# Performance work log

Measured on AMD Instinct MI355X. Metric: run time of the kernel, lower is better.

Reference implementation:

```python
import jax, jax.numpy as jnp
import numpy as np

V, DH, E, KV = 30, 512, 256, 128  # vocab, decoder hidden, embed (=2*KV, tied), key/value dim
B, T, L = 256, 800, 300
SOS = 0


def _lstm_cell(x, h, c, w_ih, w_hh, b_ih, b_hh):
    g = x @ w_ih.T + b_ih + h @ w_hh.T + b_hh
    i, f, gg, o = jnp.split(g, 4, axis=-1)
    i, f, o = jax.nn.sigmoid(i), jax.nn.sigmoid(f), jax.nn.sigmoid(o)
    c2 = f * c + i * jnp.tanh(gg)
    return o * jnp.tanh(c2), c2


def setup_inputs() -> dict:
    key = jax.random.key(0)
    ks = jax.random.split(key, 12)
    emb = 0.1 * jax.random.normal(ks[0], (V, E), jnp.float32)
    emb = emb.at[0].set(0.0)  # padding_idx=0
    return {
        "key_enc": jax.random.normal(ks[1], (B, T, KV), jnp.float32),
        "value": jax.random.normal(ks[2], (B, T, KV), jnp.float32),
        "encoder_len": jax.random.randint(ks[3], (B,), 100, T + 1, jnp.int32),
        "y": jax.random.randint(ks[4], (B, L), 0, V, jnp.int64),
        "embedding": emb,  # also the tied character_prob weight (V, 2*KV)
        "w_ih1": 0.05 * jax.random.normal(ks[5], (4 * DH, E + KV), jnp.float32),
        "w_hh1": 0.05 * jax.random.normal(ks[6], (4 * DH, DH), jnp.float32),
        "b_ih1": jnp.zeros((4 * DH,), jnp.float32),
        "b_hh1": jnp.zeros((4 * DH,), jnp.float32),
        "w_ih2": 0.05 * jax.random.normal(ks[7], (4 * KV, DH), jnp.float32),
        "w_hh2": 0.05 * jax.random.normal(ks[8], (4 * KV, KV), jnp.float32),
        "b_ih2": jnp.zeros((4 * KV,), jnp.float32),
        "b_hh2": jnp.zeros((4 * KV,), jnp.float32),
        "out_bias": jnp.zeros((V,), jnp.float32),
    }


def reference(key_enc, value, encoder_len, y, embedding,
              w_ih1, w_hh1, b_ih1, b_hh1, w_ih2, w_hh2, b_ih2, b_hh2, out_bias):
    Bb, Tt, _ = key_enc.shape
    max_len = y.shape[1]
    valid = jnp.arange(Tt)[None, :] < encoder_len[:, None]  # (B, T)

    # teacher-forced embeddings: <sos> then y[:, :-1]
    sos = jnp.broadcast_to(embedding[SOS], (Bb, E))
    embeds = jnp.concatenate([sos[:, None, :], embedding[y[:, :-1]]], axis=1)  # (B, L, E)
    embeds = jnp.transpose(embeds, (1, 0, 2))  # (L, B, E)

    z1 = jnp.zeros((Bb, DH), key_enc.dtype)
    z2 = jnp.zeros((Bb, KV), key_enc.dtype)
    init = (z1, z1, z2, z2, value[:, 0, :])

    def step(carry, emb):
        h1, c1, h2, c2, ctx = carry
        x = jnp.concatenate([emb, ctx], axis=1)
        h1, c1 = _lstm_cell(x, h1, c1, w_ih1, w_hh1, b_ih1, b_hh1)
        h2, c2 = _lstm_cell(h1, h2, c2, w_ih2, w_hh2, b_ih2, b_hh2)
        q = h2  # (B, KV)
        energy = jnp.einsum('btk,bk->bt', key_enc, q)
        energy = jnp.where(valid, energy, -1e9)
        attn = jax.nn.softmax(energy, axis=-1)
        ctx = jnp.einsum('bt,btk->bk', attn, value)
        pred = jnp.concatenate([q, ctx], axis=1) @ embedding.T + out_bias  # tied weights
        return (h1, c1, h2, c2, ctx), (pred, attn[0])

    _, (preds, attn_plot) = jax.lax.scan(step, init, embeds)
    predictions = jnp.transpose(preds, (1, 0, 2))  # (B, L, V)
    return predictions, attn_plot  # attn_plot: (L, T)
```

## Files before the change

kernel.cpp:

```cpp
#include <hip/hip_runtime.h>
#include <cstddef>

#define NV   30
#define NDH  512
#define NE   256
#define NKV  128
#define NB   256
#define NT   800
#define NL   300
#define NKX  896

#define PRED_SIZE (NB*NL*NV)

typedef float v4f __attribute__((ext_vector_type(4)));
typedef float v2f __attribute__((ext_vector_type(2)));
typedef short bf16x8 __attribute__((ext_vector_type(8)));
typedef unsigned short ushort_t;

#define OFF_XT  0
#define OFF_C1  229376
#define OFF_H2  360448
#define OFF_C2  425984
#define OFF_GP  458752
#define OFF_BP  1507328
#define OFF_XB  2031616
#define OFF_WF  2293760

struct DecParams {
  const float* key; const float* val; const int* elen; const int* y;
  const float* emb;
  const float* wi1; const float* wh1; const float* bi1; const float* bh1;
  const float* wi2; const float* wh2; const float* bi2; const float* bh2;
  const float* ob;
  float* out; float* ws;
};

__device__ __forceinline__ float sigm(float x)  { return 1.0f/(1.0f + __expf(-x)); }
__device__ __forceinline__ float tanh_f(float x){ return 1.0f - 2.0f/(__expf(2.0f*x)+1.0f); }

__device__ __forceinline__ ushort_t bf16_rne(float x){
  union { float f; unsigned u; } v; v.f = x;
  unsigned r = v.u + 0x7FFFu + ((v.u >> 16) & 1u);
  return (ushort_t)(r >> 16);
}
__device__ __forceinline__ float bf16_to_f(ushort_t h){
  union { float f; unsigned u; } v; v.u = ((unsigned)h) << 16;
  return v.f;
}

__global__ void __launch_bounds__(256)
k_init(DecParams P)
{
  const int idx = blockIdx.x * 256 + threadIdx.x;
  P.ws[idx] = 0.0f;
}

__global__ void __launch_bounds__(256)
k_initX(DecParams P)
{
  const int b = blockIdx.x, tid = threadIdx.x;
  ushort_t* xb = (ushort_t*)(P.ws + OFF_XB);
  ushort_t* xbh = xb;
  ushort_t* xbl = xb + 256*1024;
#pragma unroll
  for (int i = 0; i < 4; ++i) {
    const int k = i*256 + tid;
    float v = 0.0f;
    if (k >= 256 && k < 384) v = P.val[(size_t)b*NT*NKV + (k - 256)];
    ushort_t hi = bf16_rne(v);
    ushort_t lo = bf16_rne(v - bf16_to_f(hi));
    xbh[(size_t)b*1024 + k] = hi;
    xbl[(size_t)b*1024 + k] = lo;
  }
}

__global__ void __launch_bounds__(256)
k_initW(DecParams P)
{
  const int r = blockIdx.x;
  const int tid = threadIdx.x;
  ushort_t* wf = (ushort_t*)(P.ws + OFF_WF);
  const int rt = r >> 4;
#pragma unroll
  for (int i = 0; i < 4; ++i) {
    const int k = i*256 + tid;
    if (k < NKX) {
      const float w = (k < 384) ? P.wi1[(size_t)r*384 + k]
                                : P.wh1[(size_t)r*512 + (k - 384)];
      ushort_t hi = bf16_rne(w);
      ushort_t lo = bf16_rne(w - bf16_to_f(hi));
      const int kc = k >> 5;
      const int lane = (r & 15) | (((k >> 3) & 3) << 4);
      const int e = k & 7;
      const size_t base = ((((size_t)rt)*28 + kc)*64 + lane)*8 + e;
      wf[base] = hi;
      wf[(size_t)128*28*64*8 + base] = lo;
    }
  }
}

__global__ void __launch_bounds__(256)
k_stepA(DecParams P)
{
  __shared__ ushort_t xs[2][64][72];
  const int tid = threadIdx.x, bid = blockIdx.x;
  const int mt = bid & 31, nt = (bid >> 5) & 3, kt = bid >> 7;
  const int w = tid >> 6, lane = tid & 63;
  const int rt16 = mt*4 + w;
  const int b0 = nt * 64;

  const ushort_t* Wf = (const ushort_t*)(P.ws + OFF_WF);
  const ushort_t* Xb = (const ushort_t*)(P.ws + OFF_XB);
  float* Gp = P.ws + OFF_GP;

  v4f acc[4];
#pragma unroll
  for (int i = 0; i < 4; ++i) acc[i] = (v4f)0.0f;

  const int srow = tid >> 2, skq = (tid & 3) * 16;
  const int lr = lane & 15, lk8 = (lane >> 4) * 8;

#pragma unroll 1
  for (int p = 0; p < 7; ++p) {
    const int kg = kt*448 + p*64;
    __syncthreads();
    {
      const ushort_t* s0 = Xb + (size_t)(b0 + srow)*1024 + kg + skq;
      const ushort_t* s1 = s0 + (size_t)256*1024;
      *(bf16x8*)&xs[0][srow][skq]     = *(const bf16x8*)(s0);
      *(bf16x8*)&xs[0][srow][skq + 8] = *(const bf16x8*)(s0 + 8);
      *(bf16x8*)&xs[1][srow][skq]     = *(const bf16x8*)(s1);
      *(bf16x8*)&xs[1][srow][skq + 8] = *(const bf16x8*)(s1 + 8);
    }
    __syncthreads();
#pragma unroll
    for (int kc2 = 0; kc2 < 2; ++kc2) {
      const int kcg = (kg >> 5) + kc2;
      bf16x8 ah = *(const bf16x8*)(Wf + ((((size_t)0*128 + rt16)*28 + kcg)*64 + lane)*8);
      bf16x8 al = *(const bf16x8*)(Wf + ((((size_t)1*128 + rt16)*28 + kcg)*64 + lane)*8);
      const int lk = kc2*32 + lk8;
#pragma unroll
      for (int ct = 0; ct < 4; ++ct) {
        bf16x8 bh = *(const bf16x8*)&xs[0][ct*16 + lr][lk];
        bf16x8 bl = *(const bf16x8*)&xs[1][ct*16 + lr][lk];
        acc[ct] = __builtin_amdgcn_mfma_f32_16x16x32_bf16(ah, bh, acc[ct], 0, 0, 0);
        acc[ct] = __builtin_amdgcn_mfma_f32_16x16x32_bf16(ah, bl, acc[ct], 0, 0, 0);
        acc[ct] = __builtin_amdgcn_mfma_f32_16x16x32_bf16(al, bh, acc[ct], 0, 0, 0);
      }
    }
  }
  const int rg = (lane >> 4) * 4;
  const int r0 = rt16 * 16;
#pragma unroll
  for (int ct = 0; ct < 4; ++ct)
#pragma unroll
    for (int j = 0; j < 4; ++j)
      Gp[((size_t)kt*2048 + r0 + rg + j)*256 + b0 + ct*16 + lr] = acc[ct][j];
}

__global__ void __launch_bounds__(256)
k_afin(DecParams P)
{
  const int j = blockIdx.x;
  const int b = threadIdx.x;
  const float* Gp = P.ws + OFF_GP;
  float* Xt = P.ws + OFF_XT;
  float* C1 = P.ws + OFF_C1;
  ushort_t* xb = (ushort_t*)(P.ws + OFF_XB);

  float s[4];
#pragma unroll
  for (int g = 0; g < 4; ++g) {
    const size_t base = ((size_t)g*512 + j)*256 + b;
    s[g] = Gp[base] + Gp[(size_t)2048*256 + base]
         + P.bi1[g*512 + j] + P.bh1[g*512 + j];
  }
  const float ig = sigm(s[0]);
  const float fg = sigm(s[1]);
  const float gg = tanh_f(s[2]);
  const float og = sigm(s[3]);
  const float cn = fg * C1[(size_t)j*256 + b] + ig * gg;
  C1[(size_t)j*256 + b] = cn;
  const float h = og * tanh_f(cn);
  Xt[(size_t)(384 + j)*256 + b] = h;
  ushort_t hi = bf16_rne(h);
  ushort_t lo = bf16_rne(h - bf16_to_f(hi));
  xb[(size_t)b*1024 + 384 + j] = hi;
  xb[(size_t)256*1024 + (size_t)b*1024 + 384 + j] = lo;
}

__global__ void __launch_bounds__(256)
k_stepB(DecParams P, int t)
{
  __shared__ float xs2[32][36];
  __shared__ float wr2[32][36];
  const int tid = threadIdx.x;
  const int bid = blockIdx.x;
  const int bt = bid & 7, jt = (bid >> 3) & 15, kt = bid >> 7;
  const int b0 = bt * 32, r0 = jt * 32;
  const int bq = tid & 15, rq = tid >> 4;

  const float* Xt = P.ws + OFF_XT;
  const float* H2p = P.ws + OFF_H2 + (size_t)(t & 1) * 32768;
  float* Bp = P.ws + OFF_BP;

  v2f acc[2] = {(v2f)0.0f, (v2f)0.0f};

  const int kx_ld = tid >> 3, bx4 = (tid & 7) * 4;
  const int rw_ld = tid >> 3, kw4 = (tid & 7) * 4;

#pragma unroll 1
  for (int cc = 0; cc < 5; ++cc) {
    const int kg0 = kt * 160 + cc * 32;
    __syncthreads();
    {
      const int kg = kg0 + kx_ld;
      const float* src = (kg < 512) ? (Xt + (size_t)(384 + kg)*256 + b0 + bx4)
                                    : (H2p + (size_t)(kg - 512)*256 + b0 + bx4);
      *(v4f*)&xs2[kx_ld][bx4] = *(const v4f*)src;
    }
    {
      const int row = r0 + rw_ld;
      const int kg = kg0 + kw4;
      const float* src = (kg < 512) ? (P.wi2 + (size_t)row*512 + kg)
                                    : (P.wh2 + (size_t)row*128 + (kg - 512));
      *(v4f*)&wr2[rw_ld][kw4] = *(const v4f*)src;
    }
    __syncthreads();
#pragma unroll
    for (int p = 0; p < 16; ++p) {
      v2f x0 = *(const v2f*)&xs2[p*2+0][bq*2];
      v2f x1 = *(const v2f*)&xs2[p*2+1][bq*2];
#pragma unroll
      for (int ri = 0; ri < 2; ++ri) {
        v2f w = *(const v2f*)&wr2[rq*2+ri][p*2];
        acc[ri] += w[0]*x0 + w[1]*x1;
      }
    }
  }
#pragma unroll
  for (int bi = 0; bi < 2; ++bi) {
    v2f st; st[0] = acc[0][bi]; st[1] = acc[1][bi];
    *(v2f*)&Bp[((size_t)kt*256 + b0 + bq*2 + bi)*512 + r0 + rq*2] = st;
  }
}

__global__ void __launch_bounds__(512)
k_stepC(DecParams P, int t)
{
  __shared__ float e[NT];
  __shared__ float g2s[512];
  __shared__ float qc[256];
  __shared__ float red[16];
  __shared__ float ctxp[16][132];

  const int tid = threadIdx.x;
  const int b = blockIdx.x;
  const int len = P.elen[b];
  float* C2 = P.ws + OFF_C2;
  const float* Bp = P.ws + OFF_BP;
  float* H2n = P.ws + OFF_H2 + (size_t)((t + 1) & 1) * 32768;
  ushort_t* xbh = (ushort_t*)(P.ws + OFF_XB);
  ushort_t* xbl = xbh + (size_t)256*1024;

  {
    const int r = tid;
    const size_t base = (size_t)b*512 + r;
    float s = Bp[base] + Bp[256*512 + base] + Bp[2*256*512 + base] + Bp[3*256*512 + base]
            + P.bi2[r] + P.bh2[r];
    g2s[r] = s;
  }
  __syncthreads();
  if (tid < 128) {
    const int j2 = tid;
    const float ig = sigm(g2s[j2]);
    const float fg = sigm(g2s[128 + j2]);
    const float gg = tanh_f(g2s[256 + j2]);
    const float og = sigm(g2s[384 + j2]);
    const float cn = fg * C2[(size_t)b*128 + j2] + ig * gg;
    C2[(size_t)b*128 + j2] = cn;
    const float h = og * tanh_f(cn);
    qc[j2] = h;
    H2n[(size_t)j2*256 + b] = h;
  }
  __syncthreads();

  const int lg = tid & 15, grp = tid >> 4;
  const v4f qa = *(const v4f*)&qc[lg*8];
  const v4f qb = *(const v4f*)&qc[lg*8 + 4];
  const v4f* kb = (const v4f*)(P.key + (size_t)b*NT*NKV);
#pragma unroll 1
  for (int s = 0; s < 13; ++s) {
    const int ta = s*64 + grp, tb = ta + 32;
    float pa = 0.0f, pb = 0.0f;
    if (ta < len) {
      v4f k0 = kb[(size_t)ta*32 + lg*2], k1 = kb[(size_t)ta*32 + lg*2 + 1];
      v4f d = k0*qa + k1*qb; pa = d[0]+d[1]+d[2]+d[3];
    }
    if (tb < len) {
      v4f k0 = kb[(size_t)tb*32 + lg*2], k1 = kb[(size_t)tb*32 + lg*2 + 1];
      v4f d = k0*qa + k1*qb; pb = d[0]+d[1]+d[2]+d[3];
    }
    pa += __shfl_xor(pa, 1); pb += __shfl_xor(pb, 1);
    pa += __shfl_xor(pa, 2); pb += __shfl_xor(pb, 2);
    pa += __shfl_xor(pa, 4); pb += __shfl_xor(pb, 4);
    pa += __shfl_xor(pa, 8); pb += __shfl_xor(pb, 8);
    if (lg == 0) {
      if (ta < len) e[ta] = pa;
      if (tb < len) e[tb] = pb;
    }
  }
  for (int tt = len + tid; tt < NT; tt += 512) e[tt] = -1e9f;
  __syncthreads();

  const int wid = tid >> 6;
  const float x0 = e[tid];
  const float x1 = (tid < NT - 512) ? e[512 + tid] : -3.0e38f;
  float m = fmaxf(x0, x1);
  m = fmaxf(m, __shfl_xor(m, 1));  m = fmaxf(m, __shfl_xor(m, 2));
  m = fmaxf(m, __shfl_xor(m, 4));  m = fmaxf(m, __shfl_xor(m, 8));
  m = fmaxf(m, __shfl_xor(m, 16)); m = fmaxf(m, __shfl_xor(m, 32));
  if ((tid & 63) == 0) red[wid] = m;
  __syncthreads();
  m = red[0];
#pragma unroll
  for (int i = 1; i < 8; ++i) m = fmaxf(m, red[i]);
  const float p0 = __expf(x0 - m);
  const float p1 = (tid < NT - 512) ? __expf(x1 - m) : 0.0f;
  float ss = p0 + p1;
  ss += __shfl_xor(ss, 1);  ss += __shfl_xor(ss, 2);  ss += __shfl_xor(ss, 4);
  ss += __shfl_xor(ss, 8);  ss += __shfl_xor(ss, 16); ss += __shfl_xor(ss, 32);
  if ((tid & 63) == 0) red[8 + wid] = ss;
  __syncthreads();
  float S = red[8];
#pragma unroll
  for (int i = 1; i < 8; ++i) S += red[8 + i];
  const float inv = 1.0f / S;
  e[tid] = p0 * inv;
  if (tid < NT - 512) e[512 + tid] = p1 * inv;
  if (b == 0) {
    P.out[PRED_SIZE + (size_t)t*NT + tid] = p0 * inv;
    if (tid < NT - 512) P.out[PRED_SIZE + (size_t)t*NT + 512 + tid] = p1 * inv;
  }
  __syncthreads();

  {
    const int kq = tid & 31, tq = tid >> 5;
    const v4f* vb = (const v4f*)(P.val + (size_t)b*NT*NKV);
    v4f a4 = (v4f)0.0f, a42 = (v4f)0.0f;
    int tt = tq;
    for (; tt + 16 < len; tt += 32) {
      a4  += e[tt]      * vb[(size_t)tt*32 + kq];
      a42 += e[tt + 16] * vb[(size_t)(tt + 16)*32 + kq];
    }
    if (tt < len) a4 += e[tt] * vb[(size_t)tt*32 + kq];
    a4 += a42;
    *(v4f*)&ctxp[tq][kq*4] = a4;
  }
  __syncthreads();
  if (tid < 128) {
    const int k = tid;
    float c = 0.0f;
#pragma unroll
    for (int r = 0; r < 16; ++r) c += ctxp[r][k];
    qc[128 + k] = c;
    ushort_t hi = bf16_rne(c);
    ushort_t lo = bf16_rne(c - bf16_to_f(hi));
    xbh[(size_t)b*1024 + 256 + k] = hi;
    xbl[(size_t)b*1024 + 256 + k] = lo;
  }
  __syncthreads();

  {
    const int vv = tid >> 4, lg16 = tid & 15;
    if (vv < NV) {
      const v4f* er = (const v4f*)(P.emb + (size_t)vv*NE + lg16*16);
      const v4f* qr = (const v4f*)&qc[lg16*16];
      v4f s4 = er[0]*qr[0] + er[1]*qr[1] + er[2]*qr[2] + er[3]*qr[3];
      float p = s4[0] + s4[1] + s4[2] + s4[3];
      p += __shfl_xor(p, 1); p += __shfl_xor(p, 2);
      p += __shfl_xor(p, 4); p += __shfl_xor(p, 8);
      if (lg16 == 0) P.out[((size_t)b*NL + t)*NV + vv] = p + P.ob[vv];
    }
  }

  if (tid < 256) {
    const int tok = P.y[(size_t)b*NL + t];
    const float x = P.emb[(size_t)tok*NE + tid];
    ushort_t hi = bf16_rne(x);
    ushort_t lo = bf16_rne(x - bf16_to_f(hi));
    xbh[(size_t)b*1024 + tid] = hi;
    xbl[(size_t)b*1024 + tid] = lo;
  }
}

extern "C" void kernel_launch(void* const* d_in, const int* in_sizes, int n_in,
                              void* d_out, int out_size, void* d_ws, size_t ws_size,
                              hipStream_t stream) {
  (void)in_sizes; (void)n_in; (void)out_size; (void)ws_size;
  DecParams P;
  P.key  = (const float*)d_in[0];
  P.val  = (const float*)d_in[1];
  P.elen = (const int*)d_in[2];
  P.y    = (const int*)d_in[3];
  P.emb  = (const float*)d_in[4];
  P.wi1  = (const float*)d_in[5];
  P.wh1  = (const float*)d_in[6];
  P.bi1  = (const float*)d_in[7];
  P.bh1  = (const float*)d_in[8];
  P.wi2  = (const float*)d_in[9];
  P.wh2  = (const float*)d_in[10];
  P.bi2  = (const float*)d_in[11];
  P.bh2  = (const float*)d_in[12];
  P.ob   = (const float*)d_in[13];
  P.out  = (float*)d_out;
  P.ws   = (float*)d_ws;

  hipLaunchKernelGGL(k_init,  dim3(1792), dim3(256), 0, stream, P);
  hipLaunchKernelGGL(k_initX, dim3(256),  dim3(256), 0, stream, P);
  hipLaunchKernelGGL(k_initW, dim3(2048), dim3(256), 0, stream, P);
  for (int t = 0; t < NL; ++t) {
    hipLaunchKernelGGL(k_stepA, dim3(256), dim3(256), 0, stream, P);
    hipLaunchKernelGGL(k_afin,  dim3(512), dim3(256), 0, stream, P);
    hipLaunchKernelGGL(k_stepB, dim3(512), dim3(256), 0, stream, P, t);
    hipLaunchKernelGGL(k_stepC, dim3(NB),  dim3(512), 0, stream, P, t);
  }
}
```

Baseline: 14.94 ms.

## Fuse LSTM gate epilogues into MFMA GEMMs and move layer-2 GEMM to split-bf16 MFMA

Layer-1 GEMM no longer splits K across blocks. Each block now computes all four gates for a 16-unit by 32-batch tile and applies the LSTM cell in-kernel, which removes the separate k_afin launch and the partial-sum buffer. Layer-2 is reworked the same way: its weights are prepacked to hi/lo bf16 fragments and it uses 3-pass MFMA, and the layer-2 cell update moves out of stepC into stepB. This cuts per-step launches from four to three and drops a global round-trip. The trade-off is fewer blocks per GEMM (256 and 64), with longer K loops per block.

```diff
diff --git a/kernel.cpp b/kernel.cpp
--- a/kernel.cpp
+++ b/kernel.cpp
@@ -13,18 +13,21 @@
 #define PRED_SIZE (NB*NL*NV)
 
 typedef float v4f __attribute__((ext_vector_type(4)));
-typedef float v2f __attribute__((ext_vector_type(2)));
 typedef short bf16x8 __attribute__((ext_vector_type(8)));
 typedef unsigned short ushort_t;
 
-#define OFF_XT  0
-#define OFF_C1  229376
-#define OFF_H2  360448
-#define OFF_C2  425984
-#define OFF_GP  458752
-#define OFF_BP  1507328
-#define OFF_XB  2031616
-#define OFF_WF  2293760
+#define OFF_C1   0
+#define OFF_C2   131072
+#define OFF_H2F  163840
+#define OFF_XB   196608
+#define OFF_XH2  458752
+#define OFF_WF   524288
+#define OFF_WF2  2359296
+#define OFF_BS1  2686976
+#define OFF_BS2  2689024
+
+#define WF_PL   ((size_t)128*28*64*8)
+#define WF2_PL  ((size_t)32*20*64*8)
 
 struct DecParams {
   const float* key; const float* val; const int* elen; const int* y;
@@ -51,26 +54,21 @@
 __global__ void __launch_bounds__(256)
 k_init(DecParams P)
 {
-  const int idx = blockIdx.x * 256 + threadIdx.x;
-  P.ws[idx] = 0.0f;
+  P.ws[blockIdx.x * 256 + threadIdx.x] = 0.0f;
 }
 
 __global__ void __launch_bounds__(256)
 k_initX(DecParams P)
 {
   const int b = blockIdx.x, tid = threadIdx.x;
-  ushort_t* xb = (ushort_t*)(P.ws + OFF_XB);
-  ushort_t* xbh = xb;
-  ushort_t* xbl = xb + 256*1024;
-#pragma unroll
-  for (int i = 0; i < 4; ++i) {
-    const int k = i*256 + tid;
-    float v = 0.0f;
-    if (k >= 256 && k < 384) v = P.val[(size_t)b*NT*NKV + (k - 256)];
-    ushort_t hi = bf16_rne(v);
-    ushort_t lo = bf16_rne(v - bf16_to_f(hi));
-    xbh[(size_t)b*1024 + k] = hi;
-    xbl[(size_t)b*1024 + k] = lo;
+  if (tid < 128) {
+    ushort_t* xbh = (ushort_t*)(P.ws + OFF_XB);
+    ushort_t* xbl = xbh + (size_t)256*1024;
+    const float v = P.val[(size_t)b*NT*NKV + tid];
+    const ushort_t hi = bf16_rne(v);
+    const ushort_t lo = bf16_rne(v - bf16_to_f(hi));
+    xbh[(size_t)b*1024 + 256 + tid] = hi;
+    xbl[(size_t)b*1024 + 256 + tid] = lo;
   }
 }
 
@@ -87,60 +85,86 @@
     if (k < NKX) {
       const float w = (k < 384) ? P.wi1[(size_t)r*384 + k]
                                 : P.wh1[(size_t)r*512 + (k - 384)];
-      ushort_t hi = bf16_rne(w);
-      ushort_t lo = bf16_rne(w - bf16_to_f(hi));
+      const ushort_t hi = bf16_rne(w);
+      const ushort_t lo = bf16_rne(w - bf16_to_f(hi));
       const int kc = k >> 5;
       const int lane = (r & 15) | (((k >> 3) & 3) << 4);
       const int e = k & 7;
       const size_t base = ((((size_t)rt)*28 + kc)*64 + lane)*8 + e;
       wf[base] = hi;
-      wf[(size_t)128*28*64*8 + base] = lo;
-    }
-  }
+      wf[WF_PL + base] = lo;
+    }
+  }
+  if (tid == 0) P.ws[OFF_BS1 + r] = P.bi1[r] + P.bh1[r];
+}
+
+__global__ void __launch_bounds__(256)
+k_initW2(DecParams P)
+{
+  const int r = blockIdx.x;
+  const int tid = threadIdx.x;
+  ushort_t* wf = (ushort_t*)(P.ws + OFF_WF2);
+  const int rt = r >> 4;
+#pragma unroll
+  for (int i = 0; i < 3; ++i) {
+    const int k = i*256 + tid;
+    if (k < 640) {
+      const float w = (k < 512) ? P.wi2[(size_t)r*512 + k]
+                                : P.wh2[(size_t)r*128 + (k - 512)];
+      const ushort_t hi = bf16_rne(w);
+      const ushort_t lo = bf16_rne(w - bf16_to_f(hi));
+      const int kc = k >> 5;
+      const int lane = (r & 15) | (((k >> 3) & 3) << 4);
+      const int e = k & 7;
+      const size_t base = ((((size_t)rt)*20 + kc)*64 + lane)*8 + e;
+      wf[base] = hi;
+      wf[WF2_PL + base] = lo;
+    }
+  }
+  if (tid == 0) P.ws[OFF_BS2 + r] = P.bi2[r] + P.bh2[r];
 }
 
 __global__ void __launch_bounds__(256)
 k_stepA(DecParams P)
 {
-  __shared__ ushort_t xs[2][64][72];
+  __shared__ ushort_t xs[2][32][136];
+  __shared__ float gbuf[4][16][33];
   const int tid = threadIdx.x, bid = blockIdx.x;
-  const int mt = bid & 31, nt = (bid >> 5) & 3, kt = bid >> 7;
+  const int mt = bid & 31, nt = bid >> 5;
+  const int b0 = nt * 32, j0 = mt * 16;
   const int w = tid >> 6, lane = tid & 63;
-  const int rt16 = mt*4 + w;
-  const int b0 = nt * 64;
-
-  const ushort_t* Wf = (const ushort_t*)(P.ws + OFF_WF);
-  const ushort_t* Xb = (const ushort_t*)(P.ws + OFF_XB);
-  float* Gp = P.ws + OFF_GP;
-
-  v4f acc[4];
-#pragma unroll
-  for (int i = 0; i < 4; ++i) acc[i] = (v4f)0.0f;
-
-  const int srow = tid >> 2, skq = (tid & 3) * 16;
+  const int rt16 = w*32 + mt;
+
+  const ushort_t* Wf  = (const ushort_t*)(P.ws + OFF_WF);
+  const ushort_t* XbH = (const ushort_t*)(P.ws + OFF_XB);
+  const ushort_t* XbL = XbH + (size_t)256*1024;
+  float* C1 = P.ws + OFF_C1;
+  const float* BS1 = P.ws + OFF_BS1;
+
+  v4f acc[2] = {(v4f)0.0f, (v4f)0.0f};
+  const int srow = tid >> 3, sk = (tid & 7) * 16;
   const int lr = lane & 15, lk8 = (lane >> 4) * 8;
 
 #pragma unroll 1
   for (int p = 0; p < 7; ++p) {
-    const int kg = kt*448 + p*64;
     __syncthreads();
     {
-      const ushort_t* s0 = Xb + (size_t)(b0 + srow)*1024 + kg + skq;
-      const ushort_t* s1 = s0 + (size_t)256*1024;
-      *(bf16x8*)&xs[0][srow][skq]     = *(const bf16x8*)(s0);
-      *(bf16x8*)&xs[0][srow][skq + 8] = *(const bf16x8*)(s0 + 8);
-      *(bf16x8*)&xs[1][srow][skq]     = *(const bf16x8*)(s1);
-      *(bf16x8*)&xs[1][srow][skq + 8] = *(const bf16x8*)(s1 + 8);
+      const ushort_t* s0 = XbH + (size_t)(b0 + srow)*1024 + p*128 + sk;
+      const ushort_t* s1 = XbL + (size_t)(b0 + srow)*1024 + p*128 + sk;
+      *(bf16x8*)&xs[0][srow][sk]     = ((const bf16x8*)s0)[0];
+      *(bf16x8*)&xs[0][srow][sk + 8] = ((const bf16x8*)s0)[1];
+      *(bf16x8*)&xs[1][srow][sk]     = ((const bf16x8*)s1)[0];
+      *(bf16x8*)&xs[1][srow][sk + 8] = ((const bf16x8*)s1)[1];
     }
     __syncthreads();
 #pragma unroll
-    for (int kc2 = 0; kc2 < 2; ++kc2) {
-      const int kcg = (kg >> 5) + kc2;
-      bf16x8 ah = *(const bf16x8*)(Wf + ((((size_t)0*128 + rt16)*28 + kcg)*64 + lane)*8);
-      bf16x8 al = *(const bf16x8*)(Wf + ((((size_t)1*128 + rt16)*28 + kcg)*64 + lane)*8);
+    for (int kc2 = 0; kc2 < 4; ++kc2) {
+      const int kcg = p*4 + kc2;
+      bf16x8 ah = *(const bf16x8*)(Wf + (((size_t)rt16*28 + kcg)*64 + lane)*8);
+      bf16x8 al = *(const bf16x8*)(Wf + WF_PL + (((size_t)rt16*28 + kcg)*64 + lane)*8);
       const int lk = kc2*32 + lk8;
 #pragma unroll
-      for (int ct = 0; ct < 4; ++ct) {
+      for (int ct = 0; ct < 2; ++ct) {
         bf16x8 bh = *(const bf16x8*)&xs[0][ct*16 + lr][lk];
         bf16x8 bl = *(const bf16x8*)&xs[1][ct*16 + lr][lk];
         acc[ct] = __builtin_amdgcn_mfma_f32_16x16x32_bf16(ah, bh, acc[ct], 0, 0, 0);
@@ -149,99 +173,122 @@
       }
     }
   }
+  __syncthreads();
   const int rg = (lane >> 4) * 4;
-  const int r0 = rt16 * 16;
-#pragma unroll
-  for (int ct = 0; ct < 4; ++ct)
+#pragma unroll
+  for (int ct = 0; ct < 2; ++ct)
 #pragma unroll
     for (int j = 0; j < 4; ++j)
-      Gp[((size_t)kt*2048 + r0 + rg + j)*256 + b0 + ct*16 + lr] = acc[ct][j];
-}
-
-__global__ void __launch_bounds__(256)
-k_afin(DecParams P)
-{
-  const int j = blockIdx.x;
-  const int b = threadIdx.x;
-  const float* Gp = P.ws + OFF_GP;
-  float* Xt = P.ws + OFF_XT;
-  float* C1 = P.ws + OFF_C1;
-  ushort_t* xb = (ushort_t*)(P.ws + OFF_XB);
-
-  float s[4];
-#pragma unroll
-  for (int g = 0; g < 4; ++g) {
-    const size_t base = ((size_t)g*512 + j)*256 + b;
-    s[g] = Gp[base] + Gp[(size_t)2048*256 + base]
-         + P.bi1[g*512 + j] + P.bh1[g*512 + j];
-  }
-  const float ig = sigm(s[0]);
-  const float fg = sigm(s[1]);
-  const float gg = tanh_f(s[2]);
-  const float og = sigm(s[3]);
-  const float cn = fg * C1[(size_t)j*256 + b] + ig * gg;
-  C1[(size_t)j*256 + b] = cn;
-  const float h = og * tanh_f(cn);
-  Xt[(size_t)(384 + j)*256 + b] = h;
-  ushort_t hi = bf16_rne(h);
-  ushort_t lo = bf16_rne(h - bf16_to_f(hi));
-  xb[(size_t)b*1024 + 384 + j] = hi;
-  xb[(size_t)256*1024 + (size_t)b*1024 + 384 + j] = lo;
+      gbuf[w][rg + j][ct*16 + lr] = acc[ct][j];
+  __syncthreads();
+
+  ushort_t* XbHw = (ushort_t*)(P.ws + OFF_XB);
+  ushort_t* XbLw = XbHw + (size_t)256*1024;
+#pragma unroll
+  for (int it = 0; it < 2; ++it) {
+    const int idx = it*256 + tid;
+    const int jj = idx >> 5, bq = idx & 31;
+    const int jg = j0 + jj, b = b0 + bq;
+    const float iv = sigm (gbuf[0][jj][bq] + BS1[       jg]);
+    const float fv = sigm (gbuf[1][jj][bq] + BS1[ 512 + jg]);
+    const float gv = tanh_f(gbuf[2][jj][bq] + BS1[1024 + jg]);
+    const float ov = sigm (gbuf[3][jj][bq] + BS1[1536 + jg]);
+    const float cn = fv * C1[(size_t)jg*256 + b] + iv * gv;
+    C1[(size_t)jg*256 + b] = cn;
+    const float h = ov * tanh_f(cn);
+    const ushort_t hi = bf16_rne(h);
+    const ushort_t lo = bf16_rne(h - bf16_to_f(hi));
+    XbHw[(size_t)b*1024 + 384 + jg] = hi;
+    XbLw[(size_t)b*1024 + 384 + jg] = lo;
+  }
 }
 
 __global__ void __launch_bounds__(256)
 k_stepB(DecParams P, int t)
 {
-  __shared__ float xs2[32][36];
-  __shared__ float wr2[32][36];
-  const int tid = threadIdx.x;
-  const int bid = blockIdx.x;
-  const int bt = bid & 7, jt = (bid >> 3) & 15, kt = bid >> 7;
-  const int b0 = bt * 32, r0 = jt * 32;
-  const int bq = tid & 15, rq = tid >> 4;
-
-  const float* Xt = P.ws + OFF_XT;
-  const float* H2p = P.ws + OFF_H2 + (size_t)(t & 1) * 32768;
-  float* Bp = P.ws + OFF_BP;
-
-  v2f acc[2] = {(v2f)0.0f, (v2f)0.0f};
-
-  const int kx_ld = tid >> 3, bx4 = (tid & 7) * 4;
-  const int rw_ld = tid >> 3, kw4 = (tid & 7) * 4;
+  __shared__ ushort_t xs[2][32][136];
+  __shared__ float gbuf[4][16][33];
+  const int tid = threadIdx.x, bid = blockIdx.x;
+  const int mt = bid & 7, nt = bid >> 3;
+  const int b0 = nt * 32, j0 = mt * 16;
+  const int w = tid >> 6, lane = tid & 63;
+  const int rt16 = w*8 + mt;
+
+  const ushort_t* Wf2 = (const ushort_t*)(P.ws + OFF_WF2);
+  const ushort_t* XbH = (const ushort_t*)(P.ws + OFF_XB);
+  const ushort_t* XbL = XbH + (size_t)256*1024;
+  const ushort_t* XH2 = (const ushort_t*)(P.ws + OFF_XH2);
+  float* C2  = P.ws + OFF_C2;
+  float* H2f = P.ws + OFF_H2F;
+  const float* BS2 = P.ws + OFF_BS2;
+  const int pp = t & 1, pn = (t + 1) & 1;
+
+  v4f acc[2] = {(v4f)0.0f, (v4f)0.0f};
+  const int srow = tid >> 3, sk = (tid & 7) * 16;
+  const int lr = lane & 15, lk8 = (lane >> 4) * 8;
 
 #pragma unroll 1
-  for (int cc = 0; cc < 5; ++cc) {
-    const int kg0 = kt * 160 + cc * 32;
+  for (int p = 0; p < 5; ++p) {
     __syncthreads();
     {
-      const int kg = kg0 + kx_ld;
-      const float* src = (kg < 512) ? (Xt + (size_t)(384 + kg)*256 + b0 + bx4)
-                                    : (H2p + (size_t)(kg - 512)*256 + b0 + bx4);
-      *(v4f*)&xs2[kx_ld][bx4] = *(const v4f*)src;
-    }
-    {
-      const int row = r0 + rw_ld;
-      const int kg = kg0 + kw4;
-      const float* src = (kg < 512) ? (P.wi2 + (size_t)row*512 + kg)
-                                    : (P.wh2 + (size_t)row*128 + (kg - 512));
-      *(v4f*)&wr2[rw_ld][kw4] = *(const v4f*)src;
+      const ushort_t* s0;
+      const ushort_t* s1;
+      if (p < 4) {
+        s0 = XbH + (size_t)(b0 + srow)*1024 + 384 + p*128 + sk;
+        s1 = XbL + (size_t)(b0 + srow)*1024 + 384 + p*128 + sk;
+      } else {
+        s0 = XH2 + ((size_t)(pp*2 + 0)*256 + b0 + srow)*128 + sk;
+        s1 = XH2 + ((size_t)(pp*2 + 1)*256 + b0 + srow)*128 + sk;
+      }
+      *(bf16x8*)&xs[0][srow][sk]     = ((const bf16x8*)s0)[0];
+      *(bf16x8*)&xs[0][srow][sk + 8] = ((const bf16x8*)s0)[1];
+      *(bf16x8*)&xs[1][srow][sk]     = ((const bf16x8*)s1)[0];
+      *(bf16x8*)&xs[1][srow][sk + 8] = ((const bf16x8*)s1)[1];
     }
     __syncthreads();
 #pragma unroll
-    for (int p = 0; p < 16; ++p) {
-      v2f x0 = *(const v2f*)&xs2[p*2+0][bq*2];
-      v2f x1 = *(const v2f*)&xs2[p*2+1][bq*2];
-#pragma unroll
-      for (int ri = 0; ri < 2; ++ri) {
-        v2f w = *(const v2f*)&wr2[rq*2+ri][p*2];
-        acc[ri] += w[0]*x0 + w[1]*x1;
+    for (int kc2 = 0; kc2 < 4; ++kc2) {
+      const int kcg = p*4 + kc2;
+      bf16x8 ah = *(const bf16x8*)(Wf2 + (((size_t)rt16*20 + kcg)*64 + lane)*8);
+      bf16x8 al = *(const bf16x8*)(Wf2 + WF2_PL + (((size_t)rt16*20 + kcg)*64 + lane)*8);
+      const int lk = kc2*32 + lk8;
+#pragma unroll
+      for (int ct = 0; ct < 2; ++ct) {
+        bf16x8 bh = *(const bf16x8*)&xs[0][ct*16 + lr][lk];
+        bf16x8 bl = *(const bf16x8*)&xs[1][ct*16 + lr][lk];
+        acc[ct] = __builtin_amdgcn_mfma_f32_16x16x32_bf16(ah, bh, acc[ct], 0, 0, 0);
+        acc[ct] = __builtin_amdgcn_mfma_f32_16x16x32_bf16(ah, bl, acc[ct], 0, 0, 0);
+        acc[ct] = __builtin_amdgcn_mfma_f32_16x16x32_bf16(al, bh, acc[ct], 0, 0, 0);
       }
     }
   }
-#pragma unroll
-  for (int bi = 0; bi < 2; ++bi) {
-    v2f st; st[0] = acc[0][bi]; st[1] = acc[1][bi];
-    *(v2f*)&Bp[((size_t)kt*256 + b0 + bq*2 + bi)*512 + r0 + rq*2] = st;
+  __syncthreads();
+  const int rg = (lane >> 4) * 4;
+#pragma unroll
+  for (int ct = 0; ct < 2; ++ct)
+#pragma unroll
+    for (int j = 0; j < 4; ++j)
+      gbuf[w][rg + j][ct*16 + lr] = acc[ct][j];
+  __syncthreads();
+
+  ushort_t* XH2w = (ushort_t*)(P.ws + OFF_XH2);
+#pragma unroll
+  for (int it = 0; it < 2; ++it) {
+    const int idx = it*256 + tid;
+    const int jj = idx >> 5, bq = idx & 31;
+    const int j2 = j0 + jj, b = b0 + bq;
+    const float iv = sigm (gbuf[0][jj][bq] + BS2[      j2]);
+    const float fv = sigm (gbuf[1][jj][bq] + BS2[128 + j2]);
+    const float gv = tanh_f(gbuf[2][jj][bq] + BS2[256 + j2]);
+    const float ov = sigm (gbuf[3][jj][bq] + BS2[384 + j2]);
+    const float cn = fv * C2[(size_t)j2*256 + b] + iv * gv;
+    C2[(size_t)j2*256 + b] = cn;
+    const float h = ov * tanh_f(cn);
+    H2f[(size_t)b*128 + j2] = h;
+    const ushort_t hi = bf16_rne(h);
+    const ushort_t lo = bf16_rne(h - bf16_to_f(hi));
+    XH2w[((size_t)(pn*2 + 0)*256 + b)*128 + j2] = hi;
+    XH2w[((size_t)(pn*2 + 1)*256 + b)*128 + j2] = lo;
   }
 }
 
@@ -249,7 +296,6 @@
 k_stepC(DecParams P, int t)
 {
   __shared__ float e[NT];
-  __shared__ float g2s[512];
   __shared__ float qc[256];
   __shared__ float red[16];
   __shared__ float ctxp[16][132];
@@ -257,32 +303,11 @@
   const int tid = threadIdx.x;
   const int b = blockIdx.x;
   const int len = P.elen[b];
-  float* C2 = P.ws + OFF_C2;
-  const float* Bp = P.ws + OFF_BP;
-  float* H2n = P.ws + OFF_H2 + (size_t)((t + 1) & 1) * 32768;
+  const float* H2f = P.ws + OFF_H2F;
   ushort_t* xbh = (ushort_t*)(P.ws + OFF_XB);
   ushort_t* xbl = xbh + (size_t)256*1024;
 
-  {
-    const int r = tid;
-    const size_t base = (size_t)b*512 + r;
-    float s = Bp[base] + Bp[256*512 + base] + Bp[2*256*512 + base] + Bp[3*256*512 + base]
-            + P.bi2[r] + P.bh2[r];
-    g2s[r] = s;
-  }
-  __syncthreads();
-  if (tid < 128) {
-    const int j2 = tid;
-    const float ig = sigm(g2s[j2]);
-    const float fg = sigm(g2s[128 + j2]);
-    const float gg = tanh_f(g2s[256 + j2]);
-    const float og = sigm(g2s[384 + j2]);
-    const float cn = fg * C2[(size_t)b*128 + j2] + ig * gg;
-    C2[(size_t)b*128 + j2] = cn;
-    const float h = og * tanh_f(cn);
-    qc[j2] = h;
-    H2n[(size_t)j2*256 + b] = h;
-  }
+  if (tid < 128) qc[tid] = H2f[(size_t)b*128 + tid];
   __syncthreads();
 
   const int lg = tid & 15, grp = tid >> 4;
@@ -364,8 +389,8 @@
 #pragma unroll
     for (int r = 0; r < 16; ++r) c += ctxp[r][k];
     qc[128 + k] = c;
-    ushort_t hi = bf16_rne(c);
-    ushort_t lo = bf16_rne(c - bf16_to_f(hi));
+    const ushort_t hi = bf16_rne(c);
+    const ushort_t lo = bf16_rne(c - bf16_to_f(hi));
     xbh[(size_t)b*1024 + 256 + k] = hi;
     xbl[(size_t)b*1024 + 256 + k] = lo;
   }
@@ -387,8 +412,8 @@
   if (tid < 256) {
     const int tok = P.y[(size_t)b*NL + t];
     const float x = P.emb[(size_t)tok*NE + tid];
-    ushort_t hi = bf16_rne(x);
-    ushort_t lo = bf16_rne(x - bf16_to_f(hi));
+    const ushort_t hi = bf16_rne(x);
+    const ushort_t lo = bf16_rne(x - bf16_to_f(hi));
     xbh[(size_t)b*1024 + tid] = hi;
     xbl[(size_t)b*1024 + tid] = lo;
   }
@@ -416,13 +441,13 @@
   P.out  = (float*)d_out;
   P.ws   = (float*)d_ws;
 
-  hipLaunchKernelGGL(k_init,  dim3(1792), dim3(256), 0, stream, P);
-  hipLaunchKernelGGL(k_initX, dim3(256),  dim3(256), 0, stream, P);
-  hipLaunchKernelGGL(k_initW, dim3(2048), dim3(256), 0, stream, P);
+  hipLaunchKernelGGL(k_init,   dim3(2048), dim3(256), 0, stream, P);
+  hipLaunchKernelGGL(k_initX,  dim3(256),  dim3(256), 0, stream, P);
+  hipLaunchKernelGGL(k_initW,  dim3(2048), dim3(256), 0, stream, P);
+  hipLaunchKernelGGL(k_initW2, dim3(512),  dim3(256), 0, stream, P);
   for (int t = 0; t < NL; ++t) {
     hipLaunchKernelGGL(k_stepA, dim3(256), dim3(256), 0, stream, P);
-    hipLaunchKernelGGL(k_afin,  dim3(512), dim3(256), 0, stream, P);
-    hipLaunchKernelGGL(k_stepB, dim3(512), dim3(256), 0, stream, P, t);
+    hipLaunchKernelGGL(k_stepB, dim3(64),  dim3(256), 0, stream, P, t);
     hipLaunchKernelGGL(k_stepC, dim3(NB),  dim3(512), 0, stream, P, t);
   }
 }
```

Result: slower. 15.61 ms (+4.5%).
